# Kernel tuning notes

Measured on AMD Instinct MI355X. Metric: run time of the kernel, lower is better.

## Reference

```python
import jax, jax.numpy as jnp
import numpy as np

D_MODEL = 1024
N_HEADS = 16
HEAD_DIM = D_MODEL // N_HEADS


def setup_inputs() -> dict:
    key = jax.random.key(0)
    k1, k2, k3, k4, k5, k6 = jax.random.split(key, 6)
    B, T_q, T_kv = 4, 1024, 4096
    s = 1.0 / np.sqrt(D_MODEL)
    return {
        "query": jax.random.normal(k1, (B, T_q, D_MODEL), dtype=jnp.float32),
        "kv_source": jax.random.normal(k2, (B, T_kv, D_MODEL), dtype=jnp.float32),
        "w_q": jax.random.normal(k3, (D_MODEL, D_MODEL), dtype=jnp.float32) * s,
        "w_k": jax.random.normal(k4, (D_MODEL, D_MODEL), dtype=jnp.float32) * s,
        "w_v": jax.random.normal(k5, (D_MODEL, D_MODEL), dtype=jnp.float32) * s,
        "w_o": jax.random.normal(k6, (D_MODEL, D_MODEL), dtype=jnp.float32) * s,
    }


def reference(query, kv_source, w_q, w_k, w_v, w_o):
    B, T_q, _ = query.shape
    T_kv = kv_source.shape[1]
    # Linear(d,d,bias=False): y = x @ W^T
    q = (query @ w_q.T).reshape(B, T_q, N_HEADS, HEAD_DIM)
    k = (kv_source @ w_k.T).reshape(B, T_kv, N_HEADS, HEAD_DIM)
    v = (kv_source @ w_v.T).reshape(B, T_kv, N_HEADS, HEAD_DIM)
    scale = HEAD_DIM ** -0.5
    # scores: (B, H, T_q, T_kv)
    attn = jax.nn.softmax(jnp.einsum('bqhd,bkhd->bhqk', q, k) * scale, axis=-1)
    out = jnp.einsum('bhqk,bkhd->bqhd', attn, v).reshape(B, T_q, D_MODEL)
    return out @ w_o.T
```

## Files before the change

### kernel.cpp

```cpp
#include <hip/hip_runtime.h>


typedef __attribute__((ext_vector_type(4))) float f32x4;
typedef __attribute__((ext_vector_type(8))) short bf16x8;

__device__ __forceinline__ unsigned short f2bf(float f) {
  unsigned u = __float_as_uint(f);
  u = (u + 0x7fffu + ((u >> 16) & 1u)) >> 16;
  return (unsigned short)u;
}

#define GLD_LDS16(g, l)                                                     \
  __builtin_amdgcn_global_load_lds(                                        \
      (const __attribute__((address_space(1))) unsigned int*)(const void*)(g), \
      (__attribute__((address_space(3))) unsigned int*)(void*)(l), 16, 0, 0)

__global__ void cvt_f32_bf16(const float* __restrict__ in,
                             unsigned short* __restrict__ out, int n) {
  int stride = gridDim.x * blockDim.x * 4;
  for (int i = (blockIdx.x * blockDim.x + threadIdx.x) * 4; i < n; i += stride) {
    float4 v = *(const float4*)(in + i);
    ushort4 o;
    o.x = f2bf(v.x); o.y = f2bf(v.y); o.z = f2bf(v.z); o.w = f2bf(v.w);
    *(ushort4*)(out + i) = o;
  }
}

template <int WRITE_BF16>
__global__ __launch_bounds__(256) void gemm_bt(
    const unsigned short* __restrict__ A, const unsigned short* __restrict__ Bt,
    void* __restrict__ Cp, int M, int N, int K, int ldc) {
  __shared__ __align__(16) unsigned short Ash[4096];
  __shared__ __align__(16) unsigned short Bsh[4096];

  int tiles_n = N >> 7;
  int nwg = gridDim.x;
  int wg = blockIdx.x;
  int cpx = nwg >> 3;
  wg = (wg & 7) * cpx + (wg >> 3);
  int tm = wg / tiles_n, tn = wg - tm * tiles_n;

  int tid = threadIdx.x;
  int lane = tid & 63, wave = tid >> 6;
  int wr = wave >> 1, wc = wave & 1;
  int brow = tm << 7, bcol = tn << 7;

  int fr = lane & 15, fg = lane >> 4;
  int swz = (fr >> 1) & 3;

  int srow = lane >> 2;
  int sg = (lane & 3) ^ ((srow >> 1) & 3);

  const unsigned short* aG0 = A + (size_t)(brow + wave * 32 + srow) * K + sg * 8;
  const unsigned short* aG1 = A + (size_t)(brow + wave * 32 + 16 + srow) * K + sg * 8;
  const unsigned short* bG0 = Bt + (size_t)(bcol + wave * 32 + srow) * K + sg * 8;
  const unsigned short* bG1 = Bt + (size_t)(bcol + wave * 32 + 16 + srow) * K + sg * 8;
  unsigned short* aL0 = Ash + wave * 1024;
  unsigned short* aL1 = Ash + wave * 1024 + 512;
  unsigned short* bL0 = Bsh + wave * 1024;
  unsigned short* bL1 = Bsh + wave * 1024 + 512;

  const f32x4 zero4 = {0.f, 0.f, 0.f, 0.f};
  f32x4 acc[4][4];
#pragma unroll
  for (int m = 0; m < 4; ++m)
#pragma unroll
    for (int n = 0; n < 4; ++n) acc[m][n] = zero4;

  for (int k0 = 0; k0 < K; k0 += 32) {
    GLD_LDS16(aG0 + k0, aL0);
    GLD_LDS16(aG1 + k0, aL1);
    GLD_LDS16(bG0 + k0, bL0);
    GLD_LDS16(bG1 + k0, bL1);
    __syncthreads();

    bf16x8 af[4], bfr[4];
#pragma unroll
    for (int m = 0; m < 4; ++m) {
      int r = wr * 64 + m * 16 + fr;
      af[m] = *(const bf16x8*)(Ash + r * 32 + ((fg ^ swz) * 8));
    }
#pragma unroll
    for (int n = 0; n < 4; ++n) {
      int r = wc * 64 + n * 16 + fr;
      bfr[n] = *(const bf16x8*)(Bsh + r * 32 + ((fg ^ swz) * 8));
    }
#pragma unroll
    for (int m = 0; m < 4; ++m)
#pragma unroll
      for (int n = 0; n < 4; ++n)
        acc[m][n] =
            __builtin_amdgcn_mfma_f32_16x16x32_bf16(af[m], bfr[n], acc[m][n], 0, 0, 0);
    __syncthreads();
  }

  int crow = brow + wr * 64 + fg * 4;
  int ccol = bcol + wc * 64 + fr;
#pragma unroll
  for (int m = 0; m < 4; ++m)
#pragma unroll
    for (int n = 0; n < 4; ++n)
#pragma unroll
      for (int j = 0; j < 4; ++j) {
        size_t off = (size_t)(crow + m * 16 + j) * ldc + (ccol + n * 16);
        if (WRITE_BF16)
          ((unsigned short*)Cp)[off] = f2bf(acc[m][n][j]);
        else
          ((float*)Cp)[off] = acc[m][n][j];
      }
}

__global__ __launch_bounds__(256) void attn_fwd(
    const unsigned short* __restrict__ qp,
    const unsigned short* __restrict__ kp,
    const unsigned short* __restrict__ vt,
    unsigned short* __restrict__ ao) {
  __shared__ __align__(16) unsigned short Ksh[128 * 64];
  __shared__ __align__(16) unsigned short Vsh[64 * 128];
  __shared__ __align__(16) unsigned short Psh[4][16 * 136];

  int idx = (blockIdx.x & 7) * 128 + (blockIdx.x >> 3);
  int qt = idx & 15;
  int h = (idx >> 4) & 15;
  int b = idx >> 8;
  int tid = threadIdx.x;
  int lane = tid & 63, w = tid >> 6;
  int fr = lane & 15, fg = lane >> 4;

  const float SC = 0.125f * 1.44269504088896f;

  int qrow = b * 1024 + qt * 64 + w * 16 + fr;
  bf16x8 qf0 = *(const bf16x8*)(qp + (size_t)qrow * 1024 + h * 64 + fg * 8);
  bf16x8 qf1 = *(const bf16x8*)(qp + (size_t)qrow * 1024 + h * 64 + 32 + fg * 8);

  const f32x4 zero4 = {0.f, 0.f, 0.f, 0.f};
  f32x4 o[4];
#pragma unroll
  for (int n = 0; n < 4; ++n) o[n] = zero4;
  float m[4], ssum[4];
#pragma unroll
  for (int j = 0; j < 4; ++j) { m[j] = -1e30f; ssum[j] = 0.f; }

  int rK = w * 32 + (lane >> 3);
  int gK = (lane & 7) ^ ((lane >> 3) & 7);
  const unsigned short* ksrc = kp + (size_t)(b * 4096 + rK) * 1024 + h * 64 + gK * 8;
  const unsigned short* vsrc[4];
#pragma unroll
  for (int i = 0; i < 4; ++i) {
    int dV = w * 16 + i * 4 + (lane >> 4);
    int gV = (lane & 15) ^ ((i * 4 + (lane >> 4)) & 15);
    vsrc[i] = vt + (size_t)(h * 64 + dV) * 16384 + b * 4096 + gV * 8;
  }

  unsigned short* pw = &Psh[w][0];

  for (int kv0 = 0; kv0 < 4096; kv0 += 128) {
#pragma unroll
    for (int i = 0; i < 4; ++i)
      GLD_LDS16(ksrc + (size_t)(kv0 + i * 8) * 1024, Ksh + w * 2048 + i * 512);
#pragma unroll
    for (int i = 0; i < 4; ++i)
      GLD_LDS16(vsrc[i] + kv0, Vsh + w * 2048 + i * 512);
    __syncthreads();

    f32x4 S[8];
#pragma unroll
    for (int s = 0; s < 8; ++s) S[s] = zero4;
#pragma unroll
    for (int s = 0; s < 8; ++s) {
#pragma unroll
      for (int kk = 0; kk < 2; ++kk) {
        bf16x8 kf = *(const bf16x8*)(Ksh + (s * 16 + fr) * 64 +
                                     (((kk * 4 + fg) ^ (fr & 7)) * 8));
        S[s] = __builtin_amdgcn_mfma_f32_16x16x32_bf16(kk ? qf1 : qf0, kf, S[s],
                                                       0, 0, 0);
      }
    }

    float cm[4];
#pragma unroll
    for (int j = 0; j < 4; ++j) cm[j] = -1e30f;
#pragma unroll
    for (int s = 0; s < 8; ++s)
#pragma unroll
      for (int j = 0; j < 4; ++j) {
        S[s][j] *= SC;
        cm[j] = fmaxf(cm[j], S[s][j]);
      }
#pragma unroll
    for (int mask = 1; mask <= 8; mask <<= 1)
#pragma unroll
      for (int j = 0; j < 4; ++j) cm[j] = fmaxf(cm[j], __shfl_xor(cm[j], mask));

    float fsc[4];
#pragma unroll
    for (int j = 0; j < 4; ++j) {
      float mn = fmaxf(m[j], cm[j]);
      fsc[j] = exp2f(m[j] - mn);
      m[j] = mn;
    }

    float rs[4] = {0.f, 0.f, 0.f, 0.f};
#pragma unroll
    for (int s = 0; s < 8; ++s)
#pragma unroll
      for (int j = 0; j < 4; ++j) {
        float p = exp2f(S[s][j] - m[j]);
        rs[j] += p;
        pw[(fg * 4 + j) * 136 + s * 16 + fr] = f2bf(p);
      }
#pragma unroll
    for (int mask = 1; mask <= 8; mask <<= 1)
#pragma unroll
      for (int j = 0; j < 4; ++j) rs[j] += __shfl_xor(rs[j], mask);
#pragma unroll
    for (int j = 0; j < 4; ++j) ssum[j] = ssum[j] * fsc[j] + rs[j];
#pragma unroll
    for (int n = 0; n < 4; ++n)
#pragma unroll
      for (int j = 0; j < 4; ++j) o[n][j] *= fsc[j];

#pragma unroll
    for (int kk = 0; kk < 4; ++kk) {
      bf16x8 pa = *(const bf16x8*)(pw + fr * 136 + (kk * 4 + fg) * 8);
#pragma unroll
      for (int n = 0; n < 4; ++n) {
        bf16x8 vf = *(const bf16x8*)(Vsh + (n * 16 + fr) * 128 +
                                     (((kk * 4 + fg) ^ fr) * 8));
        o[n] = __builtin_amdgcn_mfma_f32_16x16x32_bf16(pa, vf, o[n], 0, 0, 0);
      }
    }
    __syncthreads();
  }

#pragma unroll
  for (int j = 0; j < 4; ++j) {
    float inv = 1.0f / ssum[j];
    int row = b * 1024 + qt * 64 + w * 16 + fg * 4 + j;
#pragma unroll
    for (int n = 0; n < 4; ++n)
      ao[(size_t)row * 1024 + h * 64 + n * 16 + fr] = f2bf(o[n][j] * inv);
  }
}

extern "C" void kernel_launch(void* const* d_in, const int* in_sizes, int n_in,
                              void* d_out, int out_size, void* d_ws, size_t ws_size,
                              hipStream_t stream) {
  const float* query = (const float*)d_in[0];
  const float* kvs = (const float*)d_in[1];
  const float* wq = (const float*)d_in[2];
  const float* wk = (const float*)d_in[3];
  const float* wv = (const float*)d_in[4];
  const float* wo = (const float*)d_in[5];
  float* out = (float*)d_out;
  char* ws = (char*)d_ws;
  const size_t MB = 1ull << 20;

  unsigned short* q_bf = (unsigned short*)(ws + 0 * MB);
  unsigned short* kv_bf = (unsigned short*)(ws + 8 * MB);
  unsigned short* wq_bf = (unsigned short*)(ws + 40 * MB);
  unsigned short* wk_bf = (unsigned short*)(ws + 42 * MB);
  unsigned short* wv_bf = (unsigned short*)(ws + 44 * MB);
  unsigned short* wo_bf = (unsigned short*)(ws + 46 * MB);
  unsigned short* qp = (unsigned short*)(ws + 48 * MB);
  unsigned short* kp = (unsigned short*)(ws + 56 * MB);
  unsigned short* vt = (unsigned short*)(ws + 88 * MB);
  unsigned short* ao = (unsigned short*)(ws + 120 * MB);

  cvt_f32_bf16<<<1024, 256, 0, stream>>>(query, q_bf, 4096 * 1024);
  cvt_f32_bf16<<<2048, 256, 0, stream>>>(kvs, kv_bf, 16384 * 1024);
  cvt_f32_bf16<<<256, 256, 0, stream>>>(wq, wq_bf, 1024 * 1024);
  cvt_f32_bf16<<<256, 256, 0, stream>>>(wk, wk_bf, 1024 * 1024);
  cvt_f32_bf16<<<256, 256, 0, stream>>>(wv, wv_bf, 1024 * 1024);
  cvt_f32_bf16<<<256, 256, 0, stream>>>(wo, wo_bf, 1024 * 1024);

  gemm_bt<1><<<256, 256, 0, stream>>>(q_bf, wq_bf, qp, 4096, 1024, 1024, 1024);
  gemm_bt<1><<<1024, 256, 0, stream>>>(kv_bf, wk_bf, kp, 16384, 1024, 1024, 1024);
  gemm_bt<1><<<1024, 256, 0, stream>>>(wv_bf, kv_bf, vt, 1024, 16384, 1024, 16384);

  attn_fwd<<<1024, 256, 0, stream>>>(qp, kp, vt, ao);

  gemm_bt<0><<<256, 256, 0, stream>>>(ao, wo_bf, out, 4096, 1024, 1024, 1024);
}
```

Before: 529.0 us.

## Fuse conversions, fold softmax scale into Wq, and restructure attention with 512-thread blocks

Merges the six f32-to-bf16 conversion launches into one kernel and folds the softmax scale and log2e factor into the Wq conversion, which removes the per-score multiply in attention. The attention kernel moves to 512-thread blocks covering 128 query rows, so each K/V tile loaded into LDS is shared by twice as many waves. It also computes the row sums with an MFMA against a ones vector instead of shuffle reductions, skips the rescale when no row max grows, packs the P conversion, and raises wave priority around the MFMA sections. Rounding the scale into bf16 weights slightly changes numerics, and the larger blocks halve the grid size.

```diff
diff --git a/kernel.cpp b/kernel.cpp
--- a/kernel.cpp
+++ b/kernel.cpp
@@ -1,4 +1,5 @@
 #include <hip/hip_runtime.h>
+#include <hip/hip_bf16.h>
 
 
 typedef __attribute__((ext_vector_type(4))) float f32x4;
@@ -15,14 +16,36 @@
       (const __attribute__((address_space(1))) unsigned int*)(const void*)(g), \
       (__attribute__((address_space(3))) unsigned int*)(void*)(l), 16, 0, 0)
 
-__global__ void cvt_f32_bf16(const float* __restrict__ in,
-                             unsigned short* __restrict__ out, int n) {
-  int stride = gridDim.x * blockDim.x * 4;
-  for (int i = (blockIdx.x * blockDim.x + threadIdx.x) * 4; i < n; i += stride) {
-    float4 v = *(const float4*)(in + i);
-    ushort4 o;
-    o.x = f2bf(v.x); o.y = f2bf(v.y); o.z = f2bf(v.z); o.w = f2bf(v.w);
-    *(ushort4*)(out + i) = o;
+__global__ void cvt_all(const float* __restrict__ q, const float* __restrict__ kv,
+                        const float* __restrict__ wq, const float* __restrict__ wk,
+                        const float* __restrict__ wv, const float* __restrict__ wo,
+                        unsigned short* __restrict__ q_bf,
+                        unsigned short* __restrict__ kv_bf,
+                        unsigned short* __restrict__ wq_bf,
+                        unsigned short* __restrict__ wk_bf,
+                        unsigned short* __restrict__ wv_bf,
+                        unsigned short* __restrict__ wo_bf) {
+  const int QN = 4194304, KVN = 16777216, WN = 1048576;
+  const float SC = 0.125f * 1.44269504088896f;
+  int total_quads = (QN + KVN + 4 * WN) >> 2;
+  int stride = gridDim.x * blockDim.x;
+  for (int t = blockIdx.x * blockDim.x + threadIdx.x; t < total_quads; t += stride) {
+    int i = t << 2;
+    const float* src;
+    unsigned short* dst;
+    float sc = 1.0f;
+    int off;
+    if (i < QN) { src = q; dst = q_bf; off = i; }
+    else if (i < QN + KVN) { src = kv; dst = kv_bf; off = i - QN; }
+    else if (i < QN + KVN + WN) { src = wq; dst = wq_bf; off = i - QN - KVN; sc = SC; }
+    else if (i < QN + KVN + 2 * WN) { src = wk; dst = wk_bf; off = i - QN - KVN - WN; }
+    else if (i < QN + KVN + 3 * WN) { src = wv; dst = wv_bf; off = i - QN - KVN - 2 * WN; }
+    else { src = wo; dst = wo_bf; off = i - QN - KVN - 3 * WN; }
+    float4 v = *(const float4*)(src + off);
+    ushort4 r;
+    r.x = f2bf(v.x * sc); r.y = f2bf(v.y * sc);
+    r.z = f2bf(v.z * sc); r.w = f2bf(v.w * sc);
+    *(ushort4*)(dst + off) = r;
   }
 }
 
@@ -110,29 +133,31 @@
       }
 }
 
-__global__ __launch_bounds__(256) void attn_fwd(
+__global__ __launch_bounds__(512) void attn_fwd(
     const unsigned short* __restrict__ qp,
     const unsigned short* __restrict__ kp,
     const unsigned short* __restrict__ vt,
     unsigned short* __restrict__ ao) {
   __shared__ __align__(16) unsigned short Ksh[128 * 64];
   __shared__ __align__(16) unsigned short Vsh[64 * 128];
-  __shared__ __align__(16) unsigned short Psh[4][16 * 136];
-
-  int idx = (blockIdx.x & 7) * 128 + (blockIdx.x >> 3);
-  int qt = idx & 15;
-  int h = (idx >> 4) & 15;
-  int b = idx >> 8;
+  __shared__ __align__(16) unsigned short Psh[8][16 * 72];
+
+  int idx = (blockIdx.x & 7) * 64 + (blockIdx.x >> 3);
+  int qt = idx & 7;
+  int h = (idx >> 3) & 15;
+  int b = idx >> 7;
   int tid = threadIdx.x;
   int lane = tid & 63, w = tid >> 6;
   int fr = lane & 15, fg = lane >> 4;
 
-  const float SC = 0.125f * 1.44269504088896f;
-
-  int qrow = b * 1024 + qt * 64 + w * 16 + fr;
+  int qrow = b * 1024 + qt * 128 + w * 16 + fr;
   bf16x8 qf0 = *(const bf16x8*)(qp + (size_t)qrow * 1024 + h * 64 + fg * 8);
   bf16x8 qf1 = *(const bf16x8*)(qp + (size_t)qrow * 1024 + h * 64 + 32 + fg * 8);
 
+  bf16x8 ones;
+#pragma unroll
+  for (int e = 0; e < 8; ++e) ones[e] = (short)0x3F80;
+
   const f32x4 zero4 = {0.f, 0.f, 0.f, 0.f};
   f32x4 o[4];
 #pragma unroll
@@ -141,102 +166,104 @@
 #pragma unroll
   for (int j = 0; j < 4; ++j) { m[j] = -1e30f; ssum[j] = 0.f; }
 
-  int rK = w * 32 + (lane >> 3);
+  int rK = w * 16 + (lane >> 3);
   int gK = (lane & 7) ^ ((lane >> 3) & 7);
   const unsigned short* ksrc = kp + (size_t)(b * 4096 + rK) * 1024 + h * 64 + gK * 8;
-  const unsigned short* vsrc[4];
-#pragma unroll
-  for (int i = 0; i < 4; ++i) {
-    int dV = w * 16 + i * 4 + (lane >> 4);
-    int gV = (lane & 15) ^ ((i * 4 + (lane >> 4)) & 15);
-    vsrc[i] = vt + (size_t)(h * 64 + dV) * 16384 + b * 4096 + gV * 8;
-  }
+  int dV = w * 8 + (lane >> 4);
+  int gV = (lane & 15) ^ (dV & 15);
+  int gV1 = (lane & 15) ^ ((dV + 4) & 15);
+  const unsigned short* vsrc0 = vt + (size_t)(h * 64 + dV) * 16384 + b * 4096 + gV * 8;
+  const unsigned short* vsrc1 =
+      vt + (size_t)(h * 64 + dV + 4) * 16384 + b * 4096 + gV1 * 8;
 
   unsigned short* pw = &Psh[w][0];
 
   for (int kv0 = 0; kv0 < 4096; kv0 += 128) {
-#pragma unroll
-    for (int i = 0; i < 4; ++i)
-      GLD_LDS16(ksrc + (size_t)(kv0 + i * 8) * 1024, Ksh + w * 2048 + i * 512);
-#pragma unroll
-    for (int i = 0; i < 4; ++i)
-      GLD_LDS16(vsrc[i] + kv0, Vsh + w * 2048 + i * 512);
+    GLD_LDS16(ksrc + (size_t)kv0 * 1024, Ksh + w * 1024);
+    GLD_LDS16(ksrc + (size_t)kv0 * 1024 + 8192, Ksh + w * 1024 + 512);
+    GLD_LDS16(vsrc0 + kv0, Vsh + w * 1024);
+    GLD_LDS16(vsrc1 + kv0, Vsh + w * 1024 + 512);
     __syncthreads();
 
     f32x4 S[8];
 #pragma unroll
     for (int s = 0; s < 8; ++s) S[s] = zero4;
+    __builtin_amdgcn_s_setprio(1);
 #pragma unroll
     for (int s = 0; s < 8; ++s) {
+      const unsigned short* krow = Ksh + (s * 16 + fr) * 64;
+      bf16x8 kf0 = *(const bf16x8*)(krow + ((fg ^ (fr & 7)) * 8));
+      bf16x8 kf1 = *(const bf16x8*)(krow + (((4 + fg) ^ (fr & 7)) * 8));
+      S[s] = __builtin_amdgcn_mfma_f32_16x16x32_bf16(qf0, kf0, S[s], 0, 0, 0);
+      S[s] = __builtin_amdgcn_mfma_f32_16x16x32_bf16(qf1, kf1, S[s], 0, 0, 0);
+    }
+    __builtin_amdgcn_s_setprio(0);
+
+    float cm[4];
+#pragma unroll
+    for (int j = 0; j < 4; ++j) cm[j] = S[0][j];
+#pragma unroll
+    for (int s = 1; s < 8; ++s)
+#pragma unroll
+      for (int j = 0; j < 4; ++j) cm[j] = fmaxf(cm[j], S[s][j]);
+#pragma unroll
+    for (int mask = 1; mask <= 8; mask <<= 1)
+#pragma unroll
+      for (int j = 0; j < 4; ++j) cm[j] = fmaxf(cm[j], __shfl_xor(cm[j], mask));
+
+    bool grow = (cm[0] > m[0]) | (cm[1] > m[1]) | (cm[2] > m[2]) | (cm[3] > m[3]);
+    if (__any(grow)) {
+#pragma unroll
+      for (int j = 0; j < 4; ++j) {
+        float mn = fmaxf(m[j], cm[j]);
+        float fsc = exp2f(m[j] - mn);
+        m[j] = mn;
+        ssum[j] *= fsc;
+#pragma unroll
+        for (int n = 0; n < 4; ++n) o[n][j] *= fsc;
+      }
+    }
+
+    f32x4 rsum = zero4;
+#pragma unroll
+    for (int hf = 0; hf < 2; ++hf) {
+#pragma unroll
+      for (int sp = 0; sp < 4; sp += 2) {
+        int s = hf * 4 + sp;
+#pragma unroll
+        for (int j = 0; j < 4; ++j) {
+          float p0 = exp2f(S[s][j] - m[j]);
+          float p1 = exp2f(S[s + 1][j] - m[j]);
+          __hip_bfloat162 pk = __float22bfloat162_rn(float2{p0, p1});
+          unsigned u = *reinterpret_cast<unsigned*>(&pk);
+          int base = (fg * 4 + j) * 72 + sp * 16 + fr;
+          pw[base] = (unsigned short)u;
+          pw[base + 16] = (unsigned short)(u >> 16);
+        }
+      }
+      __builtin_amdgcn_s_setprio(1);
 #pragma unroll
       for (int kk = 0; kk < 2; ++kk) {
-        bf16x8 kf = *(const bf16x8*)(Ksh + (s * 16 + fr) * 64 +
-                                     (((kk * 4 + fg) ^ (fr & 7)) * 8));
-        S[s] = __builtin_amdgcn_mfma_f32_16x16x32_bf16(kk ? qf1 : qf0, kf, S[s],
-                                                       0, 0, 0);
+        bf16x8 pa = *(const bf16x8*)(pw + fr * 72 + (kk * 4 + fg) * 8);
+        rsum = __builtin_amdgcn_mfma_f32_16x16x32_bf16(pa, ones, rsum, 0, 0, 0);
+        int g = hf * 8 + kk * 4 + fg;
+#pragma unroll
+        for (int n = 0; n < 4; ++n) {
+          bf16x8 vf = *(const bf16x8*)(Vsh + (n * 16 + fr) * 128 + ((g ^ fr) * 8));
+          o[n] = __builtin_amdgcn_mfma_f32_16x16x32_bf16(pa, vf, o[n], 0, 0, 0);
+        }
       }
-    }
-
-    float cm[4];
-#pragma unroll
-    for (int j = 0; j < 4; ++j) cm[j] = -1e30f;
-#pragma unroll
-    for (int s = 0; s < 8; ++s)
-#pragma unroll
-      for (int j = 0; j < 4; ++j) {
-        S[s][j] *= SC;
-        cm[j] = fmaxf(cm[j], S[s][j]);
-      }
-#pragma unroll
-    for (int mask = 1; mask <= 8; mask <<= 1)
-#pragma unroll
-      for (int j = 0; j < 4; ++j) cm[j] = fmaxf(cm[j], __shfl_xor(cm[j], mask));
-
-    float fsc[4];
-#pragma unroll
-    for (int j = 0; j < 4; ++j) {
-      float mn = fmaxf(m[j], cm[j]);
-      fsc[j] = exp2f(m[j] - mn);
-      m[j] = mn;
-    }
-
-    float rs[4] = {0.f, 0.f, 0.f, 0.f};
-#pragma unroll
-    for (int s = 0; s < 8; ++s)
-#pragma unroll
-      for (int j = 0; j < 4; ++j) {
-        float p = exp2f(S[s][j] - m[j]);
-        rs[j] += p;
-        pw[(fg * 4 + j) * 136 + s * 16 + fr] = f2bf(p);
-      }
-#pragma unroll
-    for (int mask = 1; mask <= 8; mask <<= 1)
-#pragma unroll
-      for (int j = 0; j < 4; ++j) rs[j] += __shfl_xor(rs[j], mask);
-#pragma unroll
-    for (int j = 0; j < 4; ++j) ssum[j] = ssum[j] * fsc[j] + rs[j];
-#pragma unroll
-    for (int n = 0; n < 4; ++n)
-#pragma unroll
-      for (int j = 0; j < 4; ++j) o[n][j] *= fsc[j];
-
-#pragma unroll
-    for (int kk = 0; kk < 4; ++kk) {
-      bf16x8 pa = *(const bf16x8*)(pw + fr * 136 + (kk * 4 + fg) * 8);
-#pragma unroll
-      for (int n = 0; n < 4; ++n) {
-        bf16x8 vf = *(const bf16x8*)(Vsh + (n * 16 + fr) * 128 +
-                                     (((kk * 4 + fg) ^ fr) * 8));
-        o[n] = __builtin_amdgcn_mfma_f32_16x16x32_bf16(pa, vf, o[n], 0, 0, 0);
-      }
-    }
+      __builtin_amdgcn_s_setprio(0);
+    }
+#pragma unroll
+    for (int j = 0; j < 4; ++j) ssum[j] += rsum[j];
     __syncthreads();
   }
 
 #pragma unroll
   for (int j = 0; j < 4; ++j) {
     float inv = 1.0f / ssum[j];
-    int row = b * 1024 + qt * 64 + w * 16 + fg * 4 + j;
+    int row = b * 1024 + qt * 128 + w * 16 + fg * 4 + j;
 #pragma unroll
     for (int n = 0; n < 4; ++n)
       ao[(size_t)row * 1024 + h * 64 + n * 16 + fr] = f2bf(o[n][j] * inv);
@@ -267,18 +294,14 @@
   unsigned short* vt = (unsigned short*)(ws + 88 * MB);
   unsigned short* ao = (unsigned short*)(ws + 120 * MB);
 
-  cvt_f32_bf16<<<1024, 256, 0, stream>>>(query, q_bf, 4096 * 1024);
-  cvt_f32_bf16<<<2048, 256, 0, stream>>>(kvs, kv_bf, 16384 * 1024);
-  cvt_f32_bf16<<<256, 256, 0, stream>>>(wq, wq_bf, 1024 * 1024);
-  cvt_f32_bf16<<<256, 256, 0, stream>>>(wk, wk_bf, 1024 * 1024);
-  cvt_f32_bf16<<<256, 256, 0, stream>>>(wv, wv_bf, 1024 * 1024);
-  cvt_f32_bf16<<<256, 256, 0, stream>>>(wo, wo_bf, 1024 * 1024);
+  cvt_all<<<2048, 256, 0, stream>>>(query, kvs, wq, wk, wv, wo, q_bf, kv_bf,
+                                    wq_bf, wk_bf, wv_bf, wo_bf);
 
   gemm_bt<1><<<256, 256, 0, stream>>>(q_bf, wq_bf, qp, 4096, 1024, 1024, 1024);
   gemm_bt<1><<<1024, 256, 0, stream>>>(kv_bf, wk_bf, kp, 16384, 1024, 1024, 1024);
   gemm_bt<1><<<1024, 256, 0, stream>>>(wv_bf, kv_bf, vt, 1024, 16384, 1024, 16384);
 
-  attn_fwd<<<1024, 256, 0, stream>>>(qp, kp, vt, ao);
+  attn_fwd<<<512, 512, 0, stream>>>(qp, kp, vt, ao);
 
   gemm_bt<0><<<256, 256, 0, stream>>>(ao, wo_bf, out, 4096, 1024, 1024, 1024);
 }
```

Result: faster. 440.6 us (-16.7%).
